# Kernel optimization log

Measured on AMD Instinct MI355X. Metric: run time of the kernel, lower is better.

Reference implementation:

```python
import jax, jax.numpy as jnp
import numpy as np

B, N, NPOINT, NSAMPLE = 8, 8192, 2048, 64
RADIUS = 0.2
C_IN = 64  # input feature channels; mlp[0]=64 -> 67 after use_xyz concat


def setup_inputs() -> dict:
    key = jax.random.key(0)
    ks = jax.random.split(key, 12)
    xyz = jax.random.uniform(ks[0], (B, N, 3), dtype=jnp.float32)
    features = jax.random.normal(ks[1], (B, N, C_IN), dtype=jnp.float32)
    inds = jax.random.randint(ks[2], (B, NPOINT), 0, N, dtype=jnp.int32)

    def mkw(k, cin, cout):
        return jax.random.normal(k, (cin, cout), jnp.float32) * (1.0 / np.sqrt(cin).astype(np.float32))

    w0 = mkw(ks[3], C_IN + 3, 64)
    w1 = mkw(ks[4], 64, 64)
    w2 = mkw(ks[5], 64, 128)
    # BN (inference) folded into per-channel scale/shift
    s0 = 1.0 + 0.1 * jax.random.normal(ks[6], (64,), jnp.float32)
    t0 = 0.1 * jax.random.normal(ks[7], (64,), jnp.float32)
    s1 = 1.0 + 0.1 * jax.random.normal(ks[8], (64,), jnp.float32)
    t1 = 0.1 * jax.random.normal(ks[9], (64,), jnp.float32)
    s2 = 1.0 + 0.1 * jax.random.normal(ks[10], (128,), jnp.float32)
    t2 = 0.1 * jax.random.normal(ks[11], (128,), jnp.float32)
    return dict(xyz=xyz, features=features, inds=inds,
                w0=w0, s0=s0, t0=t0, w1=w1, s1=s1, t1=t1, w2=w2, s2=s2, t2=t2)


def _ball_query(xyz, new_xyz):
    """First NSAMPLE point indices within RADIUS of each query; pad by repeating
    the first hit (matches CUDA ball_query semantics). xyz:(B,N,3) new_xyz:(B,S,3)."""
    nn = jnp.sum(xyz * xyz, axis=-1)            # (B,N)
    qq = jnp.sum(new_xyz * new_xyz, axis=-1)    # (B,S)
    d2 = qq[:, :, None] + nn[:, None, :] - 2.0 * jnp.einsum('bsc,bnc->bsn', new_xyz, xyz)
    within = d2 < (RADIUS * RADIUS)
    ar = jnp.arange(N, dtype=jnp.int32)
    keyed = jnp.where(within, ar[None, None, :], N)   # out-of-radius -> sentinel N
    keyed = jnp.sort(keyed, axis=-1)[:, :, :NSAMPLE]  # first hits in point order
    idx = jnp.where(keyed == N, keyed[:, :, :1], keyed)
    return jnp.minimum(idx, N - 1)


_gather = jax.vmap(lambda pts, i: pts[i])  # (N,C),(M,) -> (M,C) per batch


def reference(xyz, features, inds, w0, s0, t0, w1, s1, t1, w2, s2, t2):
    new_xyz = _gather(xyz, inds)                              # (B,S,3)
    idx = _ball_query(xyz, new_xyz)                           # (B,S,ns)
    flat = idx.reshape(B, NPOINT * NSAMPLE)
    g_xyz = _gather(xyz, flat).reshape(B, NPOINT, NSAMPLE, 3)
    g_xyz = (g_xyz - new_xyz[:, :, None, :]) / RADIUS         # normalize_xyz
    g_feat = _gather(features, flat).reshape(B, NPOINT, NSAMPLE, C_IN)
    x = jnp.concatenate([g_xyz, g_feat], axis=-1)             # (B,S,ns,C+3)
    for wgt, s, t in ((w0, s0, t0), (w1, s1, t1), (w2, s2, t2)):
        x = jax.nn.relu(jnp.einsum('bpsc,cd->bpsd', x, wgt) * s + t)
    new_features = jnp.max(x, axis=2)                         # max-pool over nsample
    return new_xyz, new_features, inds, idx
```

## Files before the change

### kernel.cpp

```cpp
#include <hip/hip_runtime.h>

#define BB 8
#define NN 8192
#define NPOINT 2048
#define NSAMPLE 64
#define CIN 64
#define RADIUS 0.2f
#define R2 (RADIUS * RADIUS)

#define OFF_NEWXYZ 0
#define OFF_FEAT (BB * NPOINT * 3)
#define OFF_INDS (OFF_FEAT + BB * NPOINT * 128)
#define OFF_IDX (OFF_INDS + BB * NPOINT)

typedef _Float16 half8 __attribute__((ext_vector_type(8)));
typedef float floatx16 __attribute__((ext_vector_type(16)));

#define P0 88
#define P1 72
#define X_LOC 0
#define H_LOC (64 * P0)
#define XH_WAVE (64 * P0 + 64 * P1)
#define WT0_S 0
#define WT1_S (64 * P0)
#define WT2_S (64 * P0 + 64 * P1)

#define QPW 8

__global__ __launch_bounds__(256) void ballq_kernel(
    const float* __restrict__ xyz, const int* __restrict__ inds,
    float* __restrict__ out) {
  const int wq = (blockIdx.x * 256 + threadIdx.x) >> 6;
  const int lane = threadIdx.x & 63;
  const int b = wq >> 11;

  const float* xb = xyz + (size_t)b * NN * 3;
  const int ind = inds[wq];
  const float cx = xb[ind * 3 + 0];
  const float cy = xb[ind * 3 + 1];
  const float cz = xb[ind * 3 + 2];

  if (lane == 0) {
    out[OFF_NEWXYZ + (size_t)wq * 3 + 0] = cx;
    out[OFF_NEWXYZ + (size_t)wq * 3 + 1] = cy;
    out[OFF_NEWXYZ + (size_t)wq * 3 + 2] = cz;
    out[OFF_INDS + wq] = (float)ind;
  }

  const float qq = cx * cx + cy * cy + cz * cz;
  float* myidx = out + OFF_IDX + (size_t)wq * NSAMPLE;

  int cnt = 0;
  for (int j0 = 0; j0 < NN; j0 += 256) {
    float px[4], py[4], pz[4];
#pragma unroll
    for (int k = 0; k < 4; ++k) {
      const float* p = xb + (size_t)(j0 + k * 64 + lane) * 3;
      px[k] = p[0];
      py[k] = p[1];
      pz[k] = p[2];
    }
#pragma unroll
    for (int k = 0; k < 4; ++k) {
      const float nn = px[k] * px[k] + py[k] * py[k] + pz[k] * pz[k];
      const float dot = cx * px[k] + cy * py[k] + cz * pz[k];
      const bool hit = (qq + nn - 2.0f * dot) < R2;
      const unsigned long long m = __ballot(hit);
      if (hit) {
        const int pos = cnt + (int)__popcll(m & ((1ull << lane) - 1ull));
        if (pos < NSAMPLE) myidx[pos] = (float)(j0 + k * 64 + lane);
      }
      cnt += (int)__popcll(m);
    }
    if (cnt >= NSAMPLE) break;
  }
  const float f0 = myidx[0];
  if (lane >= cnt) myidx[lane] = f0;
}

__global__ __launch_bounds__(128, 2) void mlp_mfma(
    const float* __restrict__ xyz, const float* __restrict__ features,
    const int* __restrict__ inds,
    const float* __restrict__ w0, const float* __restrict__ s0,
    const float* __restrict__ t0, const float* __restrict__ w1,
    const float* __restrict__ s1, const float* __restrict__ t1,
    const float* __restrict__ w2, const float* __restrict__ s2,
    const float* __restrict__ t2, float* __restrict__ out) {
  __shared__ _Float16 sm[2 * XH_WAVE];
  const int tid = threadIdx.x;
  const int w = tid >> 6;
  const int l = tid & 63;
  const int l31 = l & 31;
  const int h5 = l >> 5;
  const int koff = h5 * 8;

  {
    const int d = tid >> 1, hf = tid & 1;
    const float sd0 = s0[d], td0 = t0[d], sd1 = s1[d];
#pragma unroll
    for (int j = 0; j < 44; ++j) {
      const int c = hf * 44 + j;
      float v = 0.0f;
      if (c < 64) v = w0[(3 + c) * 64 + d] * sd0;
      else if (c < 67) v = w0[(c - 64) * 64 + d] * sd0;
      else if (c == 67) v = td0;
      sm[WT0_S + d * P0 + c] = (_Float16)v;
    }
#pragma unroll
    for (int j = 0; j < 32; ++j) {
      const int c = hf * 32 + j;
      sm[WT1_S + d * P1 + c] = (_Float16)(w1[c * 64 + d] * sd1);
    }
    const int ch = tid;
    const float sch = s2[ch];
#pragma unroll
    for (int c = 0; c < 64; ++c)
      sm[WT2_S + ch * P1 + c] = (_Float16)(w2[c * 128 + ch] * sch);
  }
  __syncthreads();

  half8 b0f[2][5], b1f[2][4], b2f[4][4];
#pragma unroll
  for (int nt = 0; nt < 2; ++nt)
#pragma unroll
    for (int ks = 0; ks < 5; ++ks)
      b0f[nt][ks] =
          *(const half8*)&sm[WT0_S + (nt * 32 + l31) * P0 + ks * 16 + koff];
#pragma unroll
  for (int nt = 0; nt < 2; ++nt)
#pragma unroll
    for (int ks = 0; ks < 4; ++ks)
      b1f[nt][ks] =
          *(const half8*)&sm[WT1_S + (nt * 32 + l31) * P1 + ks * 16 + koff];
#pragma unroll
  for (int ct = 0; ct < 4; ++ct)
#pragma unroll
    for (int ks = 0; ks < 4; ++ks)
      b2f[ct][ks] =
          *(const half8*)&sm[WT2_S + (ct * 32 + l31) * P1 + ks * 16 + koff];
  const float t1v0 = t1[l31];
  const float t1v1 = t1[32 + l31];
  float t2v[4];
#pragma unroll
  for (int ct = 0; ct < 4; ++ct) t2v[ct] = t2[ct * 32 + l31];
  __syncthreads();

  _Float16* xbuf = sm + w * XH_WAVE + X_LOC;
  _Float16* hbuf = sm + w * XH_WAVE + H_LOC;
  {
    half8 z = {};
    *(half8*)&xbuf[l * P0 + 72] = z;
  }

  const int wq0 = (blockIdx.x * 2 + w) * QPW;
#pragma unroll 1
  for (int qi = 0; qi < QPW; ++qi) {
    const int q = wq0 + qi;
    const int b = q >> 11;

    const int idxs = (int)out[OFF_IDX + (size_t)q * NSAMPLE + l];
    const float* xb = xyz + (size_t)b * NN * 3;
    const int ind = inds[q];
    const float cx = xb[ind * 3 + 0], cy = xb[ind * 3 + 1],
                cz = xb[ind * 3 + 2];
    const float ppx = xb[idxs * 3 + 0], ppy = xb[idxs * 3 + 1],
                ppz = xb[idxs * 3 + 2];
    const float4* fr =
        (const float4*)(features + ((size_t)b * NN + (size_t)idxs) * CIN);
    float4 f[16];
#pragma unroll
    for (int u = 0; u < 16; ++u) f[u] = fr[u];
#pragma unroll
    for (int u = 0; u < 8; ++u) {
      half8 hv;
      hv[0] = (_Float16)f[2 * u].x;
      hv[1] = (_Float16)f[2 * u].y;
      hv[2] = (_Float16)f[2 * u].z;
      hv[3] = (_Float16)f[2 * u].w;
      hv[4] = (_Float16)f[2 * u + 1].x;
      hv[5] = (_Float16)f[2 * u + 1].y;
      hv[6] = (_Float16)f[2 * u + 1].z;
      hv[7] = (_Float16)f[2 * u + 1].w;
      *(half8*)&xbuf[l * P0 + u * 8] = hv;
    }
    {
      half8 xv = {};
      xv[0] = (_Float16)((ppx - cx) * 5.0f);
      xv[1] = (_Float16)((ppy - cy) * 5.0f);
      xv[2] = (_Float16)((ppz - cz) * 5.0f);
      xv[3] = (_Float16)1.0f;
      *(half8*)&xbuf[l * P0 + 64] = xv;
    }

    {
      half8 xa[2][5];
#pragma unroll
      for (int st = 0; st < 2; ++st)
#pragma unroll
        for (int ks = 0; ks < 5; ++ks)
          xa[st][ks] =
              *(const half8*)&xbuf[(st * 32 + l31) * P0 + ks * 16 + koff];
#pragma unroll
      for (int nt = 0; nt < 2; ++nt)
#pragma unroll
        for (int st = 0; st < 2; ++st) {
          floatx16 acc;
#pragma unroll
          for (int i = 0; i < 16; ++i) acc[i] = 0.0f;
#pragma unroll
          for (int ks = 0; ks < 5; ++ks)
            acc = __builtin_amdgcn_mfma_f32_32x32x16_f16(xa[st][ks],
                                                         b0f[nt][ks], acc,
                                                         0, 0, 0);
#pragma unroll
          for (int reg = 0; reg < 16; ++reg) {
            const int row = st * 32 + (reg & 3) + 8 * (reg >> 2) + 4 * h5;
            hbuf[row * P1 + nt * 32 + l31] =
                (_Float16)fmaxf(acc[reg], 0.0f);
          }
        }
    }

    {
      half8 ha[2][4];
#pragma unroll
      for (int st = 0; st < 2; ++st)
#pragma unroll
        for (int ks = 0; ks < 4; ++ks)
          ha[st][ks] =
              *(const half8*)&hbuf[(st * 32 + l31) * P1 + ks * 16 + koff];
#pragma unroll
      for (int nt = 0; nt < 2; ++nt) {
        const float tt = nt ? t1v1 : t1v0;
#pragma unroll
        for (int st = 0; st < 2; ++st) {
          floatx16 acc;
#pragma unroll
          for (int i = 0; i < 16; ++i) acc[i] = 0.0f;
#pragma unroll
          for (int ks = 0; ks < 4; ++ks)
            acc = __builtin_amdgcn_mfma_f32_32x32x16_f16(ha[st][ks],
                                                         b1f[nt][ks], acc,
                                                         0, 0, 0);
#pragma unroll
          for (int reg = 0; reg < 16; ++reg) {
            const int row = st * 32 + (reg & 3) + 8 * (reg >> 2) + 4 * h5;
            xbuf[row * P0 + nt * 32 + l31] =
                (_Float16)fmaxf(acc[reg] + tt, 0.0f);
          }
        }
      }
    }

    {
      half8 h1a[2][4];
#pragma unroll
      for (int st = 0; st < 2; ++st)
#pragma unroll
        for (int ks = 0; ks < 4; ++ks)
          h1a[st][ks] =
              *(const half8*)&xbuf[(st * 32 + l31) * P0 + ks * 16 + koff];
#pragma unroll
      for (int ct = 0; ct < 4; ++ct) {
        floatx16 aA, aB;
#pragma unroll
        for (int i = 0; i < 16; ++i) {
          aA[i] = 0.0f;
          aB[i] = 0.0f;
        }
#pragma unroll
        for (int ks = 0; ks < 4; ++ks) {
          aA = __builtin_amdgcn_mfma_f32_32x32x16_f16(h1a[0][ks], b2f[ct][ks],
                                                      aA, 0, 0, 0);
          aB = __builtin_amdgcn_mfma_f32_32x32x16_f16(h1a[1][ks], b2f[ct][ks],
                                                      aB, 0, 0, 0);
        }
        float m = fmaxf(aA[0], aB[0]);
#pragma unroll
        for (int i = 1; i < 16; ++i) m = fmaxf(m, fmaxf(aA[i], aB[i]));
        float v = fmaxf(m + t2v[ct], 0.0f);
        v = fmaxf(v, __shfl_xor(v, 32, 64));
        if (l < 32) out[OFF_FEAT + (size_t)q * 128 + ct * 32 + l] = v;
      }
    }
  }
}

extern "C" void kernel_launch(void* const* d_in, const int* in_sizes, int n_in,
                              void* d_out, int out_size, void* d_ws,
                              size_t ws_size, hipStream_t stream) {
  const float* xyz = (const float*)d_in[0];
  const float* features = (const float*)d_in[1];
  const int* inds = (const int*)d_in[2];
  const float* w0 = (const float*)d_in[3];
  const float* s0 = (const float*)d_in[4];
  const float* t0 = (const float*)d_in[5];
  const float* w1 = (const float*)d_in[6];
  const float* s1 = (const float*)d_in[7];
  const float* t1 = (const float*)d_in[8];
  const float* w2 = (const float*)d_in[9];
  const float* s2 = (const float*)d_in[10];
  const float* t2 = (const float*)d_in[11];
  float* out = (float*)d_out;

  const int nquery = BB * NPOINT;
  ballq_kernel<<<nquery / 4, 256, 0, stream>>>(xyz, inds, out);
  mlp_mfma<<<nquery / (2 * QPW), 128, 0, stream>>>(
      xyz, features, inds, w0, s0, t0, w1, s1, t1, w2, s2, t2, out);
}
```

Measured before the change: 188.0 us.

## Fuse ball query into MLP kernel and use packed fp16 conversions

Removes the separate ball-query kernel and runs the radius search inside the MLP kernel, once per query, with one wave per query. The found indices stay in LDS, reusing the hidden-activation buffer, so they no longer make a round trip through global memory, and one launch is dropped. Feature conversion to fp16 now uses packed round-toward-zero converts. The risks are that the serial scan now sits in front of the MFMA work in each wave, and that round-toward-zero slightly changes the numerics.

```diff
diff --git a/kernel.cpp b/kernel.cpp
--- a/kernel.cpp
+++ b/kernel.cpp
@@ -14,6 +14,7 @@
 #define OFF_IDX (OFF_INDS + BB * NPOINT)
 
 typedef _Float16 half8 __attribute__((ext_vector_type(8)));
+typedef __fp16 f16x2 __attribute__((ext_vector_type(2)));
 typedef float floatx16 __attribute__((ext_vector_type(16)));
 
 #define P0 88
@@ -27,58 +28,7 @@
 
 #define QPW 8
 
-__global__ __launch_bounds__(256) void ballq_kernel(
-    const float* __restrict__ xyz, const int* __restrict__ inds,
-    float* __restrict__ out) {
-  const int wq = (blockIdx.x * 256 + threadIdx.x) >> 6;
-  const int lane = threadIdx.x & 63;
-  const int b = wq >> 11;
-
-  const float* xb = xyz + (size_t)b * NN * 3;
-  const int ind = inds[wq];
-  const float cx = xb[ind * 3 + 0];
-  const float cy = xb[ind * 3 + 1];
-  const float cz = xb[ind * 3 + 2];
-
-  if (lane == 0) {
-    out[OFF_NEWXYZ + (size_t)wq * 3 + 0] = cx;
-    out[OFF_NEWXYZ + (size_t)wq * 3 + 1] = cy;
-    out[OFF_NEWXYZ + (size_t)wq * 3 + 2] = cz;
-    out[OFF_INDS + wq] = (float)ind;
-  }
-
-  const float qq = cx * cx + cy * cy + cz * cz;
-  float* myidx = out + OFF_IDX + (size_t)wq * NSAMPLE;
-
-  int cnt = 0;
-  for (int j0 = 0; j0 < NN; j0 += 256) {
-    float px[4], py[4], pz[4];
-#pragma unroll
-    for (int k = 0; k < 4; ++k) {
-      const float* p = xb + (size_t)(j0 + k * 64 + lane) * 3;
-      px[k] = p[0];
-      py[k] = p[1];
-      pz[k] = p[2];
-    }
-#pragma unroll
-    for (int k = 0; k < 4; ++k) {
-      const float nn = px[k] * px[k] + py[k] * py[k] + pz[k] * pz[k];
-      const float dot = cx * px[k] + cy * py[k] + cz * pz[k];
-      const bool hit = (qq + nn - 2.0f * dot) < R2;
-      const unsigned long long m = __ballot(hit);
-      if (hit) {
-        const int pos = cnt + (int)__popcll(m & ((1ull << lane) - 1ull));
-        if (pos < NSAMPLE) myidx[pos] = (float)(j0 + k * 64 + lane);
-      }
-      cnt += (int)__popcll(m);
-    }
-    if (cnt >= NSAMPLE) break;
-  }
-  const float f0 = myidx[0];
-  if (lane >= cnt) myidx[lane] = f0;
-}
-
-__global__ __launch_bounds__(128, 2) void mlp_mfma(
+__global__ __launch_bounds__(128, 2) void fused_sa(
     const float* __restrict__ xyz, const float* __restrict__ features,
     const int* __restrict__ inds,
     const float* __restrict__ w0, const float* __restrict__ s0,
@@ -147,6 +97,7 @@
 
   _Float16* xbuf = sm + w * XH_WAVE + X_LOC;
   _Float16* hbuf = sm + w * XH_WAVE + H_LOC;
+  int* idxbuf = (int*)hbuf;
   {
     half8 z = {};
     *(half8*)&xbuf[l * P0 + 72] = z;
@@ -157,12 +108,46 @@
   for (int qi = 0; qi < QPW; ++qi) {
     const int q = wq0 + qi;
     const int b = q >> 11;
-
-    const int idxs = (int)out[OFF_IDX + (size_t)q * NSAMPLE + l];
     const float* xb = xyz + (size_t)b * NN * 3;
+
     const int ind = inds[q];
     const float cx = xb[ind * 3 + 0], cy = xb[ind * 3 + 1],
                 cz = xb[ind * 3 + 2];
+    if (l == 0) {
+      out[OFF_NEWXYZ + (size_t)q * 3 + 0] = cx;
+      out[OFF_NEWXYZ + (size_t)q * 3 + 1] = cy;
+      out[OFF_NEWXYZ + (size_t)q * 3 + 2] = cz;
+      out[OFF_INDS + q] = (float)ind;
+    }
+    const float qq = cx * cx + cy * cy + cz * cz;
+
+    int cnt = 0;
+    const float* pw = xb + (size_t)l * 3;
+#pragma unroll 1
+    for (int j0 = 0; j0 < NN; j0 += 256) {
+      const float* pj = pw + (size_t)j0 * 3;
+#pragma unroll
+      for (int k = 0; k < 4; ++k) {
+        const float px = pj[k * 192 + 0];
+        const float py = pj[k * 192 + 1];
+        const float pz = pj[k * 192 + 2];
+        const float nn_ = px * px + py * py + pz * pz;
+        const float dot = cx * px + cy * py + cz * pz;
+        const bool hit = (qq + nn_ - 2.0f * dot) < R2;
+        const unsigned long long m = __ballot(hit);
+        if (hit) {
+          const int pos = cnt + (int)__popcll(m & ((1ull << l) - 1ull));
+          if (pos < NSAMPLE) idxbuf[pos] = j0 + k * 64 + l;
+        }
+        cnt += (int)__popcll(m);
+      }
+      if (cnt >= NSAMPLE) break;
+    }
+    const int vi = idxbuf[l];
+    const int v0 = idxbuf[0];
+    const int idxs = (l < cnt) ? vi : v0;
+    out[OFF_IDX + (size_t)q * NSAMPLE + l] = (float)idxs;
+
     const float ppx = xb[idxs * 3 + 0], ppy = xb[idxs * 3 + 1],
                 ppz = xb[idxs * 3 + 2];
     const float4* fr =
@@ -172,24 +157,27 @@
     for (int u = 0; u < 16; ++u) f[u] = fr[u];
 #pragma unroll
     for (int u = 0; u < 8; ++u) {
-      half8 hv;
-      hv[0] = (_Float16)f[2 * u].x;
-      hv[1] = (_Float16)f[2 * u].y;
-      hv[2] = (_Float16)f[2 * u].z;
-      hv[3] = (_Float16)f[2 * u].w;
-      hv[4] = (_Float16)f[2 * u + 1].x;
-      hv[5] = (_Float16)f[2 * u + 1].y;
-      hv[6] = (_Float16)f[2 * u + 1].z;
-      hv[7] = (_Float16)f[2 * u + 1].w;
-      *(half8*)&xbuf[l * P0 + u * 8] = hv;
-    }
-    {
-      half8 xv = {};
-      xv[0] = (_Float16)((ppx - cx) * 5.0f);
-      xv[1] = (_Float16)((ppy - cy) * 5.0f);
-      xv[2] = (_Float16)((ppz - cz) * 5.0f);
-      xv[3] = (_Float16)1.0f;
-      *(half8*)&xbuf[l * P0 + 64] = xv;
+      union {
+        half8 v;
+        f16x2 p[4];
+      } hv;
+      hv.p[0] = __builtin_amdgcn_cvt_pkrtz(f[2 * u].x, f[2 * u].y);
+      hv.p[1] = __builtin_amdgcn_cvt_pkrtz(f[2 * u].z, f[2 * u].w);
+      hv.p[2] = __builtin_amdgcn_cvt_pkrtz(f[2 * u + 1].x, f[2 * u + 1].y);
+      hv.p[3] = __builtin_amdgcn_cvt_pkrtz(f[2 * u + 1].z, f[2 * u + 1].w);
+      *(half8*)&xbuf[l * P0 + u * 8] = hv.v;
+    }
+    {
+      union {
+        half8 v;
+        f16x2 p[4];
+      } xv;
+      xv.p[0] =
+          __builtin_amdgcn_cvt_pkrtz((ppx - cx) * 5.0f, (ppy - cy) * 5.0f);
+      xv.p[1] = __builtin_amdgcn_cvt_pkrtz((ppz - cz) * 5.0f, 1.0f);
+      xv.p[2] = __builtin_amdgcn_cvt_pkrtz(0.0f, 0.0f);
+      xv.p[3] = __builtin_amdgcn_cvt_pkrtz(0.0f, 0.0f);
+      *(half8*)&xbuf[l * P0 + 64] = xv.v;
     }
 
     {
@@ -215,8 +203,7 @@
 #pragma unroll
           for (int reg = 0; reg < 16; ++reg) {
             const int row = st * 32 + (reg & 3) + 8 * (reg >> 2) + 4 * h5;
-            hbuf[row * P1 + nt * 32 + l31] =
-                (_Float16)fmaxf(acc[reg], 0.0f);
+            hbuf[row * P1 + nt * 32 + l31] = (_Float16)fmaxf(acc[reg], 0.0f);
           }
         }
     }
@@ -304,7 +291,6 @@
   float* out = (float*)d_out;
 
   const int nquery = BB * NPOINT;
-  ballq_kernel<<<nquery / 4, 256, 0, stream>>>(xyz, inds, out);
-  mlp_mfma<<<nquery / (2 * QPW), 128, 0, stream>>>(
+  fused_sa<<<nquery / (2 * QPW), 128, 0, stream>>>(
       xyz, features, inds, w0, s0, t0, w1, s1, t1, w2, s2, t2, out);
 }
```

After: 261.2 us. +39.0%, slower.
